# Optimization experiments

Measured on AMD Instinct MI355X. Metric: run time of the kernel, lower is better.

## Reference

```python
import jax, jax.numpy as jnp
import numpy as np

N_STUDENT = 100000
N_COURSE = 20000
N_EDGES = 1000000
HIDDEN = 128


def setup_inputs() -> dict:
    key = jax.random.key(0)
    ks = jax.random.split(key, 8)
    scale = 1.0 / np.sqrt(2 * HIDDEN)
    return {
        "z_student": jax.random.normal(ks[0], (N_STUDENT, HIDDEN), dtype=jnp.float32),
        "z_course": jax.random.normal(ks[1], (N_COURSE, HIDDEN), dtype=jnp.float32),
        "row": jax.random.randint(ks[2], (N_EDGES,), 0, N_STUDENT, dtype=jnp.int64),
        "col": jax.random.randint(ks[3], (N_EDGES,), 0, N_COURSE, dtype=jnp.int64),
        "W1": jax.random.normal(ks[4], (2 * HIDDEN, HIDDEN), dtype=jnp.float32) * scale,
        "b1": jnp.zeros((HIDDEN,), dtype=jnp.float32),
        "W2": jax.random.normal(ks[5], (HIDDEN, 1), dtype=jnp.float32) * (1.0 / np.sqrt(HIDDEN)),
        "b2": jnp.zeros((1,), dtype=jnp.float32),
    }


def reference(z_student, z_course, row, col, W1, b1, W2, b2):
    # gather endpoint embeddings and concat along feature dim: [E, 2H]
    z = jnp.concatenate([z_student[row], z_course[col]], axis=-1)
    h = jax.nn.relu(z @ W1 + b1)   # [E, H]
    out = h @ W2 + b2              # [E, 1]
    return out.reshape(-1)
```

## Files before the change

kernel.cpp:

```cpp
#include <hip/hip_runtime.h>
#include <hip/hip_bf16.h>
#include <hip/hip_fp16.h>


typedef _Float16 half2v __attribute__((ext_vector_type(2)));
typedef _Float16 half8v __attribute__((ext_vector_type(8)));
typedef __fp16   fp16x2 __attribute__((ext_vector_type(2)));
typedef float    float4v __attribute__((ext_vector_type(4)));

#define NB  16
#define CAP 70000

__global__ __launch_bounds__(256) void conv_w(const float* __restrict__ W1,
                                              const float* __restrict__ W2,
                                              _Float16* __restrict__ Wt,
                                              _Float16* __restrict__ w2h,
                                              int* __restrict__ cnt) {
    int b = blockIdx.x, t = threadIdx.x;
    if (b == 8) {
        if (t < 128) w2h[t] = (_Float16)W2[t];
        if (t < 32)  cnt[t] = 0;
        return;
    }
    __shared__ _Float16 lds[32][136];
    int h = b >> 2, n0 = (b & 3) * 32;
    for (int i = 0; i < 16; ++i) {
        int idx = i * 256 + t;
        int k = idx >> 5, nn = idx & 31;
        lds[nn][k] = (_Float16)W1[(h * 128 + k) * 128 + n0 + nn];
    }
    __syncthreads();
    for (int j = 0; j < 2; ++j) {
        int idx = j * 256 + t;
        int nn = idx >> 4, kc = idx & 15;
        half8v v;
        #pragma unroll
        for (int q = 0; q < 8; ++q) v[q] = lds[nn][kc * 8 + q];
        *(half8v*)&Wt[((h * 128 + n0 + nn) * 128) + kc * 8] = v;
    }
}

__global__ __launch_bounds__(256) void gemm_u(
    const float* __restrict__ Zs, const float* __restrict__ Zc,
    const _Float16* __restrict__ Wt, const float* __restrict__ b1,
    _Float16* __restrict__ Us, _Float16* __restrict__ Uc,
    int Ms, int Mc, int nbs)
{
    __shared__ uint4 ldsW[2048];
    const int bid = blockIdx.x, t = threadIdx.x;

    const float* Z; _Float16* U; const _Float16* W; int M, m0, addB;
    if (bid < nbs) { Z = Zs; U = Us; M = Ms; m0 = bid * 64;         W = Wt;         addB = 1; }
    else           { Z = Zc; U = Uc; M = Mc; m0 = (bid - nbs) * 64; W = Wt + 16384; addB = 0; }

    const uint4* Wv = (const uint4*)W;
    #pragma unroll
    for (int i = 0; i < 8; ++i) {
        int j = i * 256 + t;
        int n = j >> 4, ch = j & 15;
        ldsW[n * 16 + (ch ^ ((n >> 3) & 7))] = Wv[j];
    }
    __syncthreads();

    const int wave = t >> 6, lane = t & 63, quad = lane >> 4, l16 = lane & 15;
    int mrow = m0 + wave * 16 + l16;
    int mload = mrow < M ? mrow : M - 1;
    const float* zrow = Z + (long)mload * 128;

    float4v acc[8];
    #pragma unroll
    for (int nt = 0; nt < 8; ++nt) acc[nt] = (float4v)(0.0f);

    #pragma unroll
    for (int c = 0; c < 4; ++c) {
        const float4v* pa = (const float4v*)(zrow + c * 32 + quad * 8);
        float4v a0 = pa[0], a1 = pa[1];
        fp16x2 p[4];
        p[0] = __builtin_amdgcn_cvt_pkrtz(a0[0], a0[1]);
        p[1] = __builtin_amdgcn_cvt_pkrtz(a0[2], a0[3]);
        p[2] = __builtin_amdgcn_cvt_pkrtz(a1[0], a1[1]);
        p[3] = __builtin_amdgcn_cvt_pkrtz(a1[2], a1[3]);
        half8v af;
        __builtin_memcpy(&af, &p[0], 16);
        const int ch = c * 4 + quad;
        #pragma unroll
        for (int nt = 0; nt < 8; ++nt) {
            const int n = l16 * 8 + nt;
            const half8v* pb = (const half8v*)&ldsW[n * 16 + (ch ^ (l16 & 7))];
            acc[nt] = __builtin_amdgcn_mfma_f32_16x16x32_f16(af, *pb, acc[nt], 0, 0, 0);
        }
    }

    float bv[8];
    if (addB) {
        const float4v* pb1 = (const float4v*)(b1 + l16 * 8);
        float4v x0 = pb1[0], x1 = pb1[1];
        bv[0]=x0[0]; bv[1]=x0[1]; bv[2]=x0[2]; bv[3]=x0[3];
        bv[4]=x1[0]; bv[5]=x1[1]; bv[6]=x1[2]; bv[7]=x1[3];
    } else {
        #pragma unroll
        for (int i = 0; i < 8; ++i) bv[i] = 0.0f;
    }

    const int rbase = m0 + wave * 16 + quad * 4;
    #pragma unroll
    for (int r = 0; r < 4; ++r) {
        int rr = rbase + r;
        if (rr < M) {
            half8v o;
            #pragma unroll
            for (int nt = 0; nt < 8; ++nt) o[nt] = (_Float16)(acc[nt][r] + bv[nt]);
            *(half8v*)&U[(long)rr * 128 + l16 * 8] = o;
        }
    }
}

__global__ __launch_bounds__(256) void bucket_scatter(
    const int* __restrict__ row, const int* __restrict__ col,
    int* __restrict__ rB, int* __restrict__ cB, int* __restrict__ pos,
    int* __restrict__ cnt, int E, float scale)
{
    __shared__ int hist[NB], base[NB], hist2[NB];
    const int t = threadIdx.x;
    if (t < NB) { hist[t] = 0; hist2[t] = 0; }
    __syncthreads();
    const long e0 = (long)blockIdx.x * 1024 + t;
    int r[4], c[4], bk[4];
    bool v[4];
    #pragma unroll
    for (int k = 0; k < 4; ++k) {
        long e = e0 + k * 256;
        v[k] = e < (long)E;
        long ee = v[k] ? e : 0;
        r[k] = __builtin_nontemporal_load(&row[ee]);
        c[k] = __builtin_nontemporal_load(&col[ee]);
        int b = (int)((float)r[k] * scale);
        bk[k] = b > NB - 1 ? NB - 1 : b;
        if (v[k]) atomicAdd(&hist[bk[k]], 1);
    }
    __syncthreads();
    if (t < NB) base[t] = atomicAdd(&cnt[t], hist[t]);
    __syncthreads();
    #pragma unroll
    for (int k = 0; k < 4; ++k) {
        if (!v[k]) continue;
        int o = atomicAdd(&hist2[bk[k]], 1);
        int slot = base[bk[k]] + o;
        long e = e0 + k * 256;
        if (slot < CAP) {
            int g = bk[k] * CAP + slot;
            rB[g] = r[k];
            cB[g] = c[k];
            __builtin_nontemporal_store(g, &pos[e]);
        } else {
            __builtin_nontemporal_store(-1, &pos[e]);
        }
    }
}

__global__ __launch_bounds__(256) void edge_bucket(
    const int* __restrict__ rB, const int* __restrict__ cB,
    const int* __restrict__ cnt,
    const _Float16* __restrict__ us, const _Float16* __restrict__ uc,
    const _Float16* __restrict__ w2h, const float* __restrict__ b2,
    float* __restrict__ outB)
{
    const int t = threadIdx.x, sub = t & 7;
    const int b = blockIdx.x & (NB - 1);
    const int j = blockIdx.x >> 4;
    int n = cnt[b]; n = n < CAP ? n : CAP;
    const int seg = b * CAP;

    const uint4* pw = (const uint4*)(w2h + sub * 16);
    uint4 w0 = pw[0], w1 = pw[1];
    half2v W[8];
    *(uint4*)&W[0] = w0; *(uint4*)&W[4] = w1;
    const float bb = b2[0];
    const half2v zero = {(_Float16)0, (_Float16)0};

    for (int i0 = j * 32; i0 < n; i0 += 128 * 32) {
        int i = i0 + (t >> 3);
        bool act = i < n;
        int ii = act ? i : n - 1;
        int r = __builtin_nontemporal_load(&rB[seg + ii]);
        int c = __builtin_nontemporal_load(&cB[seg + ii]);
        const uint4* pa = (const uint4*)(us + (long)r * 128 + sub * 16);
        const uint4* pb = (const uint4*)(uc + (long)c * 128 + sub * 16);
        uint4 a0 = pa[0], a1 = pa[1];
        uint4 c0 = pb[0], c1 = pb[1];
        half2v A[8], B[8];
        *(uint4*)&A[0] = a0; *(uint4*)&A[4] = a1;
        *(uint4*)&B[0] = c0; *(uint4*)&B[4] = c1;
        float s = 0.0f;
        #pragma unroll
        for (int q = 0; q < 8; ++q) {
            half2v h = A[q] + B[q];
            h = __builtin_elementwise_max(h, zero);
            s += (float)h[0] * (float)W[q][0];
            s += (float)h[1] * (float)W[q][1];
        }
        s += __shfl_xor(s, 1);
        s += __shfl_xor(s, 2);
        s += __shfl_xor(s, 4);
        if (sub == 0 && act) outB[seg + i] = s + bb;
    }
}

__global__ __launch_bounds__(256) void unscatter(
    const int* __restrict__ pos, const float* __restrict__ outB,
    const int* __restrict__ row, const int* __restrict__ col,
    const _Float16* __restrict__ us, const _Float16* __restrict__ uc,
    const _Float16* __restrict__ w2h, const float* __restrict__ b2,
    float* __restrict__ out, int E)
{
    const int t = threadIdx.x;
    #pragma unroll
    for (int k = 0; k < 4; ++k) {
        long e = (long)blockIdx.x * 1024 + k * 256 + t;
        if (e >= (long)E) return;
        int p = pos[e];
        if (p >= 0) {
            __builtin_nontemporal_store(outB[p], &out[e]);
        } else {
            int r = row[e], c = col[e];
            float s = b2[0];
            for (int kk = 0; kk < 128; ++kk) {
                float h = (float)us[(long)r * 128 + kk] + (float)uc[(long)c * 128 + kk];
                s += fmaxf(h, 0.0f) * (float)w2h[kk];
            }
            out[e] = s;
        }
    }
}

__global__ __launch_bounds__(256) void edge_kernel(
    const int* __restrict__ row, const int* __restrict__ col,
    const _Float16* __restrict__ us, const _Float16* __restrict__ uc,
    const _Float16* __restrict__ w2h, const float* __restrict__ b2,
    float* __restrict__ out, int E)
{
    const int t = threadIdx.x;
    const int sub = t & 7;
    long e = (long)blockIdx.x * 32 + (t >> 3);
    if (e >= E) return;
    int r = row[e], c = col[e];

    const uint4* pa = (const uint4*)(us  + (long)r * 128 + sub * 16);
    const uint4* pb = (const uint4*)(uc  + (long)c * 128 + sub * 16);
    const uint4* pw = (const uint4*)(w2h + sub * 16);
    uint4 a0 = pa[0], a1 = pa[1];
    uint4 c0 = pb[0], c1 = pb[1];
    uint4 w0 = pw[0], w1 = pw[1];

    half2v A[8], B[8], W[8];
    *(uint4*)&A[0] = a0; *(uint4*)&A[4] = a1;
    *(uint4*)&B[0] = c0; *(uint4*)&B[4] = c1;
    *(uint4*)&W[0] = w0; *(uint4*)&W[4] = w1;

    const half2v zero = {(_Float16)0, (_Float16)0};
    float s = 0.0f;
    #pragma unroll
    for (int i = 0; i < 8; ++i) {
        half2v h = A[i] + B[i];
        h = __builtin_elementwise_max(h, zero);
        s += (float)h[0] * (float)W[i][0];
        s += (float)h[1] * (float)W[i][1];
    }
    s += __shfl_xor(s, 1);
    s += __shfl_xor(s, 2);
    s += __shfl_xor(s, 4);
    if (sub == 0) out[e] = s + b2[0];
}

extern "C" void kernel_launch(void* const* d_in, const int* in_sizes, int n_in,
                              void* d_out, int out_size, void* d_ws, size_t ws_size,
                              hipStream_t stream) {
    const float* zs  = (const float*)d_in[0];
    const float* zc  = (const float*)d_in[1];
    const int*   row = (const int*)d_in[2];
    const int*   col = (const int*)d_in[3];
    const float* W1  = (const float*)d_in[4];
    const float* b1  = (const float*)d_in[5];
    const float* W2  = (const float*)d_in[6];
    const float* b2  = (const float*)d_in[7];
    float* out = (float*)d_out;

    const int Ms = in_sizes[0] / 128;
    const int Mc = in_sizes[1] / 128;
    const int E  = in_sizes[2];

    char* wsb = (char*)d_ws;
    _Float16* Wt  = (_Float16*)wsb;
    _Float16* w2h = (_Float16*)(wsb + 65536);
    int*      cnt = (int*)(wsb + 65792);
    size_t off = 66048;
    _Float16* us = (_Float16*)(wsb + off);  off += (size_t)Ms * 256;
    _Float16* uc = (_Float16*)(wsb + off);  off += (size_t)Mc * 256;
    int* rB    = (int*)(wsb + off);  off += (size_t)NB * CAP * 4;
    int* cB    = (int*)(wsb + off);  off += (size_t)NB * CAP * 4;
    int* pos   = (int*)(wsb + off);  off += (size_t)E * 4;
    float* outB = (float*)(wsb + off); off += (size_t)NB * CAP * 4;
    const bool bucketed = (off <= ws_size);

    const int nbs = (Ms + 63) / 64, nbc = (Mc + 63) / 64;

    conv_w<<<9, 256, 0, stream>>>(W1, W2, Wt, w2h, cnt);
    gemm_u<<<nbs + nbc, 256, 0, stream>>>(zs, zc, Wt, b1, us, uc, Ms, Mc, nbs);
    if (bucketed) {
        bucket_scatter<<<(E + 1023) / 1024, 256, 0, stream>>>(
            row, col, rB, cB, pos, cnt, E, (float)NB / (float)Ms);
        edge_bucket<<<NB * 128, 256, 0, stream>>>(rB, cB, cnt, us, uc, w2h, b2, outB);
        unscatter<<<(E + 1023) / 1024, 256, 0, stream>>>(
            pos, outB, row, col, us, uc, w2h, b2, out, E);
    } else {
        edge_kernel<<<(E + 31) / 32, 256, 0, stream>>>(row, col, us, uc, w2h, b2, out, E);
    }
    (void)n_in; (void)out_size;
}
```

Measured before the change: 182.9 us.

## Drop unscatter pass by storing edge ids and scattering outputs directly

Replaces the pos/outB indirection and the separate unscatter kernel with a per-bucket edge-id array, so edge_bucket writes results straight to out[e]. Overflow edges are now computed inline in bucket_scatter. Buckets go from 16 to 64 with smaller capacity, so each bucket's student rows cover a smaller slice of the table and fit better in cache, and blocks now loop over 8 buckets each. This removes one launch and a full pass over pos and outB, at the cost of scattered output stores and a higher chance of bucket overflow falling to the slow scalar path.

```diff
diff --git a/kernel.cpp b/kernel.cpp
--- a/kernel.cpp
+++ b/kernel.cpp
@@ -8,8 +8,8 @@
 typedef __fp16   fp16x2 __attribute__((ext_vector_type(2)));
 typedef float    float4v __attribute__((ext_vector_type(4)));
 
-#define NB  16
-#define CAP 70000
+#define NB  64
+#define CAP 17408
 
 __global__ __launch_bounds__(256) void conv_w(const float* __restrict__ W1,
                                               const float* __restrict__ W2,
@@ -19,7 +19,7 @@
     int b = blockIdx.x, t = threadIdx.x;
     if (b == 8) {
         if (t < 128) w2h[t] = (_Float16)W2[t];
-        if (t < 32)  cnt[t] = 0;
+        if (t < NB)  cnt[t] = 0;
         return;
     }
     __shared__ _Float16 lds[32][136];
@@ -117,8 +117,11 @@
 
 __global__ __launch_bounds__(256) void bucket_scatter(
     const int* __restrict__ row, const int* __restrict__ col,
-    int* __restrict__ rB, int* __restrict__ cB, int* __restrict__ pos,
-    int* __restrict__ cnt, int E, float scale)
+    int* __restrict__ rB, int* __restrict__ cB, int* __restrict__ eB,
+    int* __restrict__ cnt, int E, float scale,
+    const _Float16* __restrict__ us, const _Float16* __restrict__ uc,
+    const _Float16* __restrict__ w2h, const float* __restrict__ b2,
+    float* __restrict__ out)
 {
     __shared__ int hist[NB], base[NB], hist2[NB];
     const int t = threadIdx.x;
@@ -151,25 +154,28 @@
             int g = bk[k] * CAP + slot;
             rB[g] = r[k];
             cB[g] = c[k];
-            __builtin_nontemporal_store(g, &pos[e]);
+            eB[g] = (int)e;
         } else {
-            __builtin_nontemporal_store(-1, &pos[e]);
+            float s = b2[0];
+            for (int kk = 0; kk < 128; ++kk) {
+                float h = (float)us[(long)r[k] * 128 + kk] + (float)uc[(long)c[k] * 128 + kk];
+                s += fmaxf(h, 0.0f) * (float)w2h[kk];
+            }
+            out[e] = s;
         }
     }
 }
 
 __global__ __launch_bounds__(256) void edge_bucket(
     const int* __restrict__ rB, const int* __restrict__ cB,
-    const int* __restrict__ cnt,
+    const int* __restrict__ eB, const int* __restrict__ cnt,
     const _Float16* __restrict__ us, const _Float16* __restrict__ uc,
     const _Float16* __restrict__ w2h, const float* __restrict__ b2,
-    float* __restrict__ outB)
+    float* __restrict__ out)
 {
     const int t = threadIdx.x, sub = t & 7;
-    const int b = blockIdx.x & (NB - 1);
-    const int j = blockIdx.x >> 4;
-    int n = cnt[b]; n = n < CAP ? n : CAP;
-    const int seg = b * CAP;
+    const int x = blockIdx.x & 7;
+    const int l = blockIdx.x >> 3;
 
     const uint4* pw = (const uint4*)(w2h + sub * 16);
     uint4 w0 = pw[0], w1 = pw[1];
@@ -178,57 +184,40 @@
     const float bb = b2[0];
     const half2v zero = {(_Float16)0, (_Float16)0};
 
-    for (int i0 = j * 32; i0 < n; i0 += 128 * 32) {
-        int i = i0 + (t >> 3);
-        bool act = i < n;
-        int ii = act ? i : n - 1;
-        int r = __builtin_nontemporal_load(&rB[seg + ii]);
-        int c = __builtin_nontemporal_load(&cB[seg + ii]);
-        const uint4* pa = (const uint4*)(us + (long)r * 128 + sub * 16);
-        const uint4* pb = (const uint4*)(uc + (long)c * 128 + sub * 16);
-        uint4 a0 = pa[0], a1 = pa[1];
-        uint4 c0 = pb[0], c1 = pb[1];
-        half2v A[8], B[8];
-        *(uint4*)&A[0] = a0; *(uint4*)&A[4] = a1;
-        *(uint4*)&B[0] = c0; *(uint4*)&B[4] = c1;
-        float s = 0.0f;
-        #pragma unroll
-        for (int q = 0; q < 8; ++q) {
-            half2v h = A[q] + B[q];
-            h = __builtin_elementwise_max(h, zero);
-            s += (float)h[0] * (float)W[q][0];
-            s += (float)h[1] * (float)W[q][1];
-        }
-        s += __shfl_xor(s, 1);
-        s += __shfl_xor(s, 2);
-        s += __shfl_xor(s, 4);
-        if (sub == 0 && act) outB[seg + i] = s + bb;
-    }
-}
-
-__global__ __launch_bounds__(256) void unscatter(
-    const int* __restrict__ pos, const float* __restrict__ outB,
-    const int* __restrict__ row, const int* __restrict__ col,
-    const _Float16* __restrict__ us, const _Float16* __restrict__ uc,
-    const _Float16* __restrict__ w2h, const float* __restrict__ b2,
-    float* __restrict__ out, int E)
-{
-    const int t = threadIdx.x;
-    #pragma unroll
-    for (int k = 0; k < 4; ++k) {
-        long e = (long)blockIdx.x * 1024 + k * 256 + t;
-        if (e >= (long)E) return;
-        int p = pos[e];
-        if (p >= 0) {
-            __builtin_nontemporal_store(outB[p], &out[e]);
-        } else {
-            int r = row[e], c = col[e];
-            float s = b2[0];
-            for (int kk = 0; kk < 128; ++kk) {
-                float h = (float)us[(long)r * 128 + kk] + (float)uc[(long)c * 128 + kk];
-                s += fmaxf(h, 0.0f) * (float)w2h[kk];
+    #pragma unroll 1
+    for (int bl = 0; bl < NB / 8; ++bl) {
+        const int b = x * (NB / 8) + bl;
+        int n = cnt[b]; n = n < CAP ? n : CAP;
+        const int seg = b * CAP;
+        #pragma unroll 1
+        for (int i0 = l * 32; i0 < n; i0 += 256 * 32) {
+            int i = i0 + (t >> 3);
+            bool act = i < n;
+            int ii = act ? i : 0;
+            int r = __builtin_nontemporal_load(&rB[seg + ii]);
+            int c = __builtin_nontemporal_load(&cB[seg + ii]);
+            const uint4* pa = (const uint4*)(us + (long)r * 128 + sub * 16);
+            const uint4* pb = (const uint4*)(uc + (long)c * 128 + sub * 16);
+            uint4 a0 = pa[0], a1 = pa[1];
+            uint4 c0 = pb[0], c1 = pb[1];
+            half2v A[8], B[8];
+            *(uint4*)&A[0] = a0; *(uint4*)&A[4] = a1;
+            *(uint4*)&B[0] = c0; *(uint4*)&B[4] = c1;
+            float s = 0.0f;
+            #pragma unroll
+            for (int q = 0; q < 8; ++q) {
+                half2v h = A[q] + B[q];
+                h = __builtin_elementwise_max(h, zero);
+                s += (float)h[0] * (float)W[q][0];
+                s += (float)h[1] * (float)W[q][1];
             }
-            out[e] = s;
+            s += __shfl_xor(s, 1);
+            s += __shfl_xor(s, 2);
+            s += __shfl_xor(s, 4);
+            if (sub == 0 && act) {
+                int e = __builtin_nontemporal_load(&eB[seg + ii]);
+                __builtin_nontemporal_store(s + bb, &out[e]);
+            }
         }
     }
 }
@@ -296,10 +285,9 @@
     size_t off = 66048;
     _Float16* us = (_Float16*)(wsb + off);  off += (size_t)Ms * 256;
     _Float16* uc = (_Float16*)(wsb + off);  off += (size_t)Mc * 256;
-    int* rB    = (int*)(wsb + off);  off += (size_t)NB * CAP * 4;
-    int* cB    = (int*)(wsb + off);  off += (size_t)NB * CAP * 4;
-    int* pos   = (int*)(wsb + off);  off += (size_t)E * 4;
-    float* outB = (float*)(wsb + off); off += (size_t)NB * CAP * 4;
+    int* rB = (int*)(wsb + off);  off += (size_t)NB * CAP * 4;
+    int* cB = (int*)(wsb + off);  off += (size_t)NB * CAP * 4;
+    int* eB = (int*)(wsb + off);  off += (size_t)NB * CAP * 4;
     const bool bucketed = (off <= ws_size);
 
     const int nbs = (Ms + 63) / 64, nbc = (Mc + 63) / 64;
@@ -308,10 +296,9 @@
     gemm_u<<<nbs + nbc, 256, 0, stream>>>(zs, zc, Wt, b1, us, uc, Ms, Mc, nbs);
     if (bucketed) {
         bucket_scatter<<<(E + 1023) / 1024, 256, 0, stream>>>(
-            row, col, rB, cB, pos, cnt, E, (float)NB / (float)Ms);
-        edge_bucket<<<NB * 128, 256, 0, stream>>>(rB, cB, cnt, us, uc, w2h, b2, outB);
-        unscatter<<<(E + 1023) / 1024, 256, 0, stream>>>(
-            pos, outB, row, col, us, uc, w2h, b2, out, E);
+            row, col, rB, cB, eB, cnt, E, (float)NB / (float)Ms,
+            us, uc, w2h, b2, out);
+        edge_bucket<<<2048, 256, 0, stream>>>(rB, cB, eB, cnt, us, uc, w2h, b2, out);
     } else {
         edge_kernel<<<(E + 31) / 32, 256, 0, stream>>>(row, col, us, uc, w2h, b2, out, E);
     }
```

New measurement: 197.8 us. +8.2%, slower.

## Use 64 finer row buckets with replicated counters and packed row/col pairs

Applied to the files above, without the earlier changes.

Raises the bucket count from 16 to 64 so each bucket's student rows form a smaller working set that fits better in cache, and splits each bucket into 8 replicas keyed by scatter block to spread global atomic contention. Row and col indices are packed into one 64-bit store/load. The edge kernel maps blocks to an XCD-like (x, replica, worker) pattern that walks several buckets per block. Per-replica capacity is small (2176), so skewed inputs could overflow more often into the slow scalar fallback in unscatter.

```diff
diff --git a/kernel.cpp b/kernel.cpp
--- a/kernel.cpp
+++ b/kernel.cpp
@@ -8,8 +8,9 @@
 typedef __fp16   fp16x2 __attribute__((ext_vector_type(2)));
 typedef float    float4v __attribute__((ext_vector_type(4)));
 
-#define NB  16
-#define CAP 70000
+#define NB   64
+#define NR   8
+#define CAPS 2176
 
 __global__ __launch_bounds__(256) void conv_w(const float* __restrict__ W1,
                                               const float* __restrict__ W2,
@@ -19,7 +20,7 @@
     int b = blockIdx.x, t = threadIdx.x;
     if (b == 8) {
         if (t < 128) w2h[t] = (_Float16)W2[t];
-        if (t < 32)  cnt[t] = 0;
+        for (int i = t; i < NB * NR; i += 256) cnt[i] = 0;
         return;
     }
     __shared__ _Float16 lds[32][136];
@@ -117,11 +118,12 @@
 
 __global__ __launch_bounds__(256) void bucket_scatter(
     const int* __restrict__ row, const int* __restrict__ col,
-    int* __restrict__ rB, int* __restrict__ cB, int* __restrict__ pos,
+    long* __restrict__ rcB, int* __restrict__ pos,
     int* __restrict__ cnt, int E, float scale)
 {
     __shared__ int hist[NB], base[NB], hist2[NB];
     const int t = threadIdx.x;
+    const int rep = blockIdx.x & (NR - 1);
     if (t < NB) { hist[t] = 0; hist2[t] = 0; }
     __syncthreads();
     const long e0 = (long)blockIdx.x * 1024 + t;
@@ -139,7 +141,7 @@
         if (v[k]) atomicAdd(&hist[bk[k]], 1);
     }
     __syncthreads();
-    if (t < NB) base[t] = atomicAdd(&cnt[t], hist[t]);
+    if (t < NB) base[t] = atomicAdd(&cnt[t * NR + rep], hist[t]);
     __syncthreads();
     #pragma unroll
     for (int k = 0; k < 4; ++k) {
@@ -147,29 +149,28 @@
         int o = atomicAdd(&hist2[bk[k]], 1);
         int slot = base[bk[k]] + o;
         long e = e0 + k * 256;
-        if (slot < CAP) {
-            int g = bk[k] * CAP + slot;
-            rB[g] = r[k];
-            cB[g] = c[k];
-            __builtin_nontemporal_store(g, &pos[e]);
-        } else {
-            __builtin_nontemporal_store(-1, &pos[e]);
-        }
+        int p = -1;
+        if (slot < CAPS) {
+            int g = (bk[k] * NR + rep) * CAPS + slot;
+            long packed = ((long)(unsigned)r[k]) | (((long)(unsigned)c[k]) << 32);
+            __builtin_nontemporal_store(packed, &rcB[g]);
+            p = g;
+        }
+        __builtin_nontemporal_store(p, &pos[e]);
     }
 }
 
 __global__ __launch_bounds__(256) void edge_bucket(
-    const int* __restrict__ rB, const int* __restrict__ cB,
-    const int* __restrict__ cnt,
+    const long* __restrict__ rcB, const int* __restrict__ cnt,
     const _Float16* __restrict__ us, const _Float16* __restrict__ uc,
     const _Float16* __restrict__ w2h, const float* __restrict__ b2,
     float* __restrict__ outB)
 {
     const int t = threadIdx.x, sub = t & 7;
-    const int b = blockIdx.x & (NB - 1);
-    const int j = blockIdx.x >> 4;
-    int n = cnt[b]; n = n < CAP ? n : CAP;
-    const int seg = b * CAP;
+    const int x = blockIdx.x & 7;
+    const int l = blockIdx.x >> 3;
+    const int p = l & 7;
+    const int w = l >> 3;
 
     const uint4* pw = (const uint4*)(w2h + sub * 16);
     uint4 w0 = pw[0], w1 = pw[1];
@@ -178,31 +179,40 @@
     const float bb = b2[0];
     const half2v zero = {(_Float16)0, (_Float16)0};
 
-    for (int i0 = j * 32; i0 < n; i0 += 128 * 32) {
-        int i = i0 + (t >> 3);
-        bool act = i < n;
-        int ii = act ? i : n - 1;
-        int r = __builtin_nontemporal_load(&rB[seg + ii]);
-        int c = __builtin_nontemporal_load(&cB[seg + ii]);
-        const uint4* pa = (const uint4*)(us + (long)r * 128 + sub * 16);
-        const uint4* pb = (const uint4*)(uc + (long)c * 128 + sub * 16);
-        uint4 a0 = pa[0], a1 = pa[1];
-        uint4 c0 = pb[0], c1 = pb[1];
-        half2v A[8], B[8];
-        *(uint4*)&A[0] = a0; *(uint4*)&A[4] = a1;
-        *(uint4*)&B[0] = c0; *(uint4*)&B[4] = c1;
-        float s = 0.0f;
-        #pragma unroll
-        for (int q = 0; q < 8; ++q) {
-            half2v h = A[q] + B[q];
-            h = __builtin_elementwise_max(h, zero);
-            s += (float)h[0] * (float)W[q][0];
-            s += (float)h[1] * (float)W[q][1];
-        }
-        s += __shfl_xor(s, 1);
-        s += __shfl_xor(s, 2);
-        s += __shfl_xor(s, 4);
-        if (sub == 0 && act) outB[seg + i] = s + bb;
+    #pragma unroll 1
+    for (int bl = 0; bl < NB / 8; ++bl) {
+        const int b = x * (NB / 8) + bl;
+        const int ss = b * NR + p;
+        int n = cnt[ss]; n = n < CAPS ? n : CAPS;
+        const int seg = ss * CAPS;
+        #pragma unroll 1
+        for (int i0 = w * 32; i0 < n; i0 += 32 * 32) {
+            int i = i0 + (t >> 3);
+            bool act = i < n;
+            int ii = act ? i : 0;
+            long rc = __builtin_nontemporal_load(&rcB[seg + ii]);
+            int r = (int)(rc & 0xffffffffL);
+            int c = (int)(rc >> 32);
+            const uint4* pa = (const uint4*)(us + (long)r * 128 + sub * 16);
+            const uint4* pb = (const uint4*)(uc + (long)c * 128 + sub * 16);
+            uint4 a0 = pa[0], a1 = pa[1];
+            uint4 c0 = pb[0], c1 = pb[1];
+            half2v A[8], B[8];
+            *(uint4*)&A[0] = a0; *(uint4*)&A[4] = a1;
+            *(uint4*)&B[0] = c0; *(uint4*)&B[4] = c1;
+            float s = 0.0f;
+            #pragma unroll
+            for (int q = 0; q < 8; ++q) {
+                half2v h = A[q] + B[q];
+                h = __builtin_elementwise_max(h, zero);
+                s += (float)h[0] * (float)W[q][0];
+                s += (float)h[1] * (float)W[q][1];
+            }
+            s += __shfl_xor(s, 1);
+            s += __shfl_xor(s, 2);
+            s += __shfl_xor(s, 4);
+            if (sub == 0 && act) outB[seg + i] = s + bb;
+        }
     }
 }
 
@@ -218,18 +228,19 @@
     for (int k = 0; k < 4; ++k) {
         long e = (long)blockIdx.x * 1024 + k * 256 + t;
         if (e >= (long)E) return;
-        int p = pos[e];
+        int p = __builtin_nontemporal_load(&pos[e]);
+        float s;
         if (p >= 0) {
-            __builtin_nontemporal_store(outB[p], &out[e]);
+            s = outB[p];
         } else {
             int r = row[e], c = col[e];
-            float s = b2[0];
+            s = b2[0];
             for (int kk = 0; kk < 128; ++kk) {
                 float h = (float)us[(long)r * 128 + kk] + (float)uc[(long)c * 128 + kk];
                 s += fmaxf(h, 0.0f) * (float)w2h[kk];
             }
-            out[e] = s;
-        }
+        }
+        __builtin_nontemporal_store(s, &out[e]);
     }
 }
 
@@ -293,13 +304,12 @@
     _Float16* Wt  = (_Float16*)wsb;
     _Float16* w2h = (_Float16*)(wsb + 65536);
     int*      cnt = (int*)(wsb + 65792);
-    size_t off = 66048;
+    size_t off = 67840;
     _Float16* us = (_Float16*)(wsb + off);  off += (size_t)Ms * 256;
     _Float16* uc = (_Float16*)(wsb + off);  off += (size_t)Mc * 256;
-    int* rB    = (int*)(wsb + off);  off += (size_t)NB * CAP * 4;
-    int* cB    = (int*)(wsb + off);  off += (size_t)NB * CAP * 4;
-    int* pos   = (int*)(wsb + off);  off += (size_t)E * 4;
-    float* outB = (float*)(wsb + off); off += (size_t)NB * CAP * 4;
+    long*  rcB  = (long*)(wsb + off);  off += (size_t)NB * NR * CAPS * 8;
+    int*   pos  = (int*)(wsb + off);   off += (size_t)E * 4;
+    float* outB = (float*)(wsb + off); off += (size_t)NB * NR * CAPS * 4;
     const bool bucketed = (off <= ws_size);
 
     const int nbs = (Ms + 63) / 64, nbc = (Mc + 63) / 64;
@@ -308,8 +318,8 @@
     gemm_u<<<nbs + nbc, 256, 0, stream>>>(zs, zc, Wt, b1, us, uc, Ms, Mc, nbs);
     if (bucketed) {
         bucket_scatter<<<(E + 1023) / 1024, 256, 0, stream>>>(
-            row, col, rB, cB, pos, cnt, E, (float)NB / (float)Ms);
-        edge_bucket<<<NB * 128, 256, 0, stream>>>(rB, cB, cnt, us, uc, w2h, b2, outB);
+            row, col, rcB, pos, cnt, E, (float)NB / (float)Ms);
+        edge_bucket<<<2048, 256, 0, stream>>>(rcB, cnt, us, uc, w2h, b2, outB);
         unscatter<<<(E + 1023) / 1024, 256, 0, stream>>>(
             pos, outB, row, col, us, uc, w2h, b2, out, E);
     } else {
```

Result: slower. 190.2 us (+4.0%).
